# Kernel optimization log

Hardware: AMD Instinct MI355X
Metric: run time of the kernel (lower is better)

## Reference

```python
import jax, jax.numpy as jnp
import numpy as np

ALPHA = 0.15
N_PROPAGATION = 5
N_NODES = 100000
N_EDGES = 1600000
N_CLASSES = 50


def setup_inputs() -> dict:
    key = jax.random.key(0)
    k1, k2, k3, k4 = jax.random.split(key, 4)
    logits = jax.random.normal(k1, (N_NODES, N_CLASSES), dtype=jnp.float32)
    edge_rows = jax.random.randint(k2, (N_EDGES,), 0, N_NODES, dtype=jnp.int32)
    edge_cols = jax.random.randint(k3, (N_EDGES,), 0, N_NODES, dtype=jnp.int32)
    edge_vals = jax.random.uniform(k4, (N_EDGES,), dtype=jnp.float32)
    return {"logits": logits, "edge_rows": edge_rows, "edge_cols": edge_cols,
            "edge_vals": edge_vals}


def reference(logits, edge_rows, edge_cols, edge_vals):
    """APPNP-style power iteration: logits <- alpha*init + (1-alpha)*A_hat@logits.

    A_hat is given as an edge list (rows=dest, cols=src, vals=weights).
    Note: the source module's per-step dropout is dead code (its result is
    discarded and the original A_hat is used in the spmm), so the effective
    math carries no dropout.
    """
    n = logits.shape[0]
    initial_logits = logits

    def step(l, _):
        # sparse A_hat @ l: gather source rows, scale by edge value, scatter-add to dest
        msg = edge_vals[:, None] * l[edge_cols]          # [E, C]
        agg = jax.ops.segment_sum(msg, edge_rows, num_segments=n)  # [N, C]
        return ALPHA * initial_logits + (1.0 - ALPHA) * agg, None

    out, _ = jax.lax.scan(step, logits, None, length=N_PROPAGATION)
    return out
```

## Files before the change

### kernel.cpp

```cpp
#include <hip/hip_runtime.h>


constexpr float ALPHA  = 0.15f;
constexpr int   NPROP  = 5;
constexpr int   NCLASS = 50;
constexpr int   C2     = 25;
constexpr int   C2P    = 32;
constexpr int   NPB    = 10;
constexpr int   NB     = 256;
constexpr int   PB     = 256;
constexpr int   RBSH   = 9;

__device__ __forceinline__ unsigned f2bf(float x) {
    unsigned u = __float_as_uint(x);
    return (u + 0x7fffu + ((u >> 16) & 1u)) >> 16;
}


__global__ __launch_bounds__(256) void reduce_chunk(const int* __restrict__ counts,
                                                    int* __restrict__ bs, int n) {
    __shared__ int tsum[256];
    int b = blockIdx.x, t = threadIdx.x;
    int chunk = (n + gridDim.x - 1) / gridDim.x;
    int blo = b * chunk;
    int bhi = blo + chunk; if (bhi > n) bhi = n;
    int s = 0;
    for (int i = blo + t; i < bhi; i += 256) s += counts[i];
    tsum[t] = s;
    __syncthreads();
    for (int off = 128; off; off >>= 1) {
        if (t < off) tsum[t] += tsum[t + off];
        __syncthreads();
    }
    if (t == 0) bs[b] = tsum[0];
}

__global__ __launch_bounds__(256) void scan_blocksums(int* __restrict__ bs) {
    __shared__ int tmp[256];
    int t = threadIdx.x;
    tmp[t] = bs[t];
    __syncthreads();
    for (int off = 1; off < 256; off <<= 1) {
        int v = (t >= off) ? tmp[t - off] : 0;
        __syncthreads();
        tmp[t] += v;
        __syncthreads();
    }
    bs[t] = t ? tmp[t - 1] : 0;
}

__global__ __launch_bounds__(256) void scan_chunk(int* __restrict__ counts,
                                                  const int* __restrict__ bs,
                                                  int* __restrict__ offs,
                                                  int n, int E) {
    __shared__ int tsum[256];
    int b = blockIdx.x, t = threadIdx.x;
    int chunk = (n + gridDim.x - 1) / gridDim.x;
    int blo = b * chunk;
    int bhi = blo + chunk; if (bhi > n) bhi = n;
    int per = (chunk + 255) / 256;
    int lo = blo + t * per;
    int hi = lo + per;
    if (lo > bhi) lo = bhi;
    if (hi > bhi) hi = bhi;
    int s = 0;
    for (int i = lo; i < hi; ++i) s += counts[i];
    tsum[t] = s;
    __syncthreads();
    for (int off = 1; off < 256; off <<= 1) {
        int v = (t >= off) ? tsum[t - off] : 0;
        __syncthreads();
        tsum[t] += v;
        __syncthreads();
    }
    int run = bs[b] + (t ? tsum[t - 1] : 0);
    for (int i = lo; i < hi; ++i) {
        int v = counts[i];
        offs[i] = run;
        run += v;
    }
    if (b == 0 && t == 0) offs[n] = E;
}


__global__ __launch_bounds__(256) void part_hist(const int* __restrict__ rows,
                                                 int* __restrict__ blockhist, int E) {
    __shared__ int h[NB];
    int b = blockIdx.x, t = threadIdx.x;
    h[t] = 0;
    __syncthreads();
    int chunk = (E + gridDim.x - 1) / gridDim.x;
    int lo = b * chunk;
    int hi = lo + chunk; if (hi > E) hi = E;
    for (int i = lo + t; i < hi; i += 256) atomicAdd(&h[rows[i] >> RBSH], 1);
    __syncthreads();
    blockhist[t * PB + b] = h[t];
}

__global__ __launch_bounds__(256) void part_scatter(const int* __restrict__ rows,
                                                    const int* __restrict__ cols,
                                                    const float* __restrict__ vals,
                                                    const int* __restrict__ bh_scanned,
                                                    int2* __restrict__ recbuf, int E) {
    __shared__ int cur[NB];
    int b = blockIdx.x, t = threadIdx.x;
    cur[t] = bh_scanned[t * PB + b];
    __syncthreads();
    int chunk = (E + gridDim.x - 1) / gridDim.x;
    int lo = b * chunk;
    int hi = lo + chunk; if (hi > E) hi = E;
    for (int i = lo + t; i < hi; i += 256) {
        int r  = rows[i];
        int bk = r >> RBSH;
        int p  = atomicAdd(&cur[bk], 1);
        int2 rec;
        rec.x = ((r & ((1 << RBSH) - 1)) << 17) | cols[i];
        rec.y = __float_as_int(vals[i]);
        recbuf[p] = rec;
    }
}

__global__ __launch_bounds__(256) void bucket_csr(const int2* __restrict__ recbuf,
                                                  const int* __restrict__ bh_scanned,
                                                  int* __restrict__ offs,
                                                  int2* __restrict__ epack,
                                                  int N, int E) {
    __shared__ int cnt[512];
    __shared__ int ex[512];
    __shared__ int pair[256];
    int b = blockIdx.x, t = threadIdx.x;
    int rowlo = b << RBSH;
    int nrows = N - rowlo; if (nrows > (1 << RBSH)) nrows = (1 << RBSH);
    int bstart = bh_scanned[b * PB];
    int bend   = (b == gridDim.x - 1) ? E : bh_scanned[(b + 1) * PB];

    cnt[t] = 0; cnt[t + 256] = 0;
    __syncthreads();
    for (int k = bstart + t; k < bend; k += 256)
        atomicAdd(&cnt[recbuf[k].x >> 17], 1);
    __syncthreads();

    int c0 = cnt[2 * t], c1 = cnt[2 * t + 1];
    pair[t] = c0 + c1;
    __syncthreads();
    for (int off = 1; off < 256; off <<= 1) {
        int v = (t >= off) ? pair[t - off] : 0;
        __syncthreads();
        pair[t] += v;
        __syncthreads();
    }
    int pbase = t ? pair[t - 1] : 0;
    ex[2 * t]     = pbase;
    ex[2 * t + 1] = pbase + c0;
    __syncthreads();

    if (t < nrows)        offs[rowlo + t]       = bstart + ex[t];
    if (t + 256 < nrows)  offs[rowlo + t + 256] = bstart + ex[t + 256];
    if (t == 0 && rowlo + nrows == N) offs[N] = E;

    for (int k = bstart + t; k < bend; k += 256) {
        int2 rec = recbuf[k];
        int lr  = rec.x >> 17;
        int col = rec.x & 0x1FFFF;
        int p   = bstart + atomicAdd(&ex[lr], 1);
        int2 e; e.x = col; e.y = rec.y;
        epack[p] = e;
    }
}


__global__ __launch_bounds__(256) void to_bf16_kernel(const float* __restrict__ logits,
                                                      unsigned* __restrict__ lbf, int N) {
    int i = blockIdx.x * blockDim.x + threadIdx.x;
    int stride = gridDim.x * blockDim.x;
    int total = N << 5;
    const float2* l2 = (const float2*)logits;
    for (; i < total; i += stride) {
        int node = i >> 5;
        int c = i & 31;
        unsigned v = 0;
        if (c < C2) {
            float2 lv = l2[node * C2 + c];
            v = f2bf(lv.x) | (f2bf(lv.y) << 16);
        }
        lbf[i] = v;
    }
}


__global__ __launch_bounds__(256) void spmm_bf_kernel(
    const unsigned* __restrict__ lbf, const float* __restrict__ init,
    const int* __restrict__ offs, const int2* __restrict__ epack,
    unsigned* __restrict__ obf, float* __restrict__ of32, int n, int final_f32) {
    int t = threadIdx.x;
    if (t >= NPB * C2) return;
    int node = blockIdx.x * NPB + t / C2;
    if (node >= n) return;
    int c = t % C2;
    int beg = offs[node], end = offs[node + 1];
    float ax0 = 0.f, ay0 = 0.f, ax1 = 0.f, ay1 = 0.f;
    int k = beg;
    for (; k + 4 <= end; k += 4) {
        int2 e0 = epack[k];
        int2 e1 = epack[k + 1];
        int2 e2 = epack[k + 2];
        int2 e3 = epack[k + 3];
        unsigned u0 = lbf[(e0.x << 5) + c];
        unsigned u1 = lbf[(e1.x << 5) + c];
        unsigned u2 = lbf[(e2.x << 5) + c];
        unsigned u3 = lbf[(e3.x << 5) + c];
        float v0 = __int_as_float(e0.y);
        float v1 = __int_as_float(e1.y);
        float v2 = __int_as_float(e2.y);
        float v3 = __int_as_float(e3.y);
        ax0 = fmaf(v0, __uint_as_float(u0 << 16), ax0);
        ay0 = fmaf(v0, __uint_as_float(u0 & 0xffff0000u), ay0);
        ax1 = fmaf(v1, __uint_as_float(u1 << 16), ax1);
        ay1 = fmaf(v1, __uint_as_float(u1 & 0xffff0000u), ay1);
        ax0 = fmaf(v2, __uint_as_float(u2 << 16), ax0);
        ay0 = fmaf(v2, __uint_as_float(u2 & 0xffff0000u), ay0);
        ax1 = fmaf(v3, __uint_as_float(u3 << 16), ax1);
        ay1 = fmaf(v3, __uint_as_float(u3 & 0xffff0000u), ay1);
    }
    for (; k < end; ++k) {
        int2 e = epack[k];
        unsigned u = lbf[(e.x << 5) + c];
        float v = __int_as_float(e.y);
        ax0 = fmaf(v, __uint_as_float(u << 16), ax0);
        ay0 = fmaf(v, __uint_as_float(u & 0xffff0000u), ay0);
    }
    float ax = ax0 + ax1, ay = ay0 + ay1;
    float2 iv = ((const float2*)init)[node * C2 + c];
    float ox = ALPHA * iv.x + (1.0f - ALPHA) * ax;
    float oy = ALPHA * iv.y + (1.0f - ALPHA) * ay;
    if (final_f32) {
        float2 o; o.x = ox; o.y = oy;
        ((float2*)of32)[node * C2 + c] = o;
    } else {
        obf[(node << 5) + c] = f2bf(ox) | (f2bf(oy) << 16);
    }
}


__global__ void zero_f32(float* __restrict__ p, int n) {
    int i = blockIdx.x * blockDim.x + threadIdx.x;
    int stride = gridDim.x * blockDim.x;
    for (; i < n; i += stride) p[i] = 0.0f;
}

__global__ __launch_bounds__(256) void scatter_kernel(
    const float* __restrict__ l, const int* __restrict__ rows,
    const int* __restrict__ cols, const float* __restrict__ vals,
    float* __restrict__ agg, int E) {
    long long gid = (long long)blockIdx.x * blockDim.x + threadIdx.x;
    int e = (int)(gid >> 6);
    if (e >= E) return;
    int c = (int)(gid & 63);
    if (c >= NCLASS) return;
    float m = vals[e] * l[(long long)cols[e] * NCLASS + c];
    atomicAdd(&agg[(long long)rows[e] * NCLASS + c], m);
}

__global__ void combine_kernel(const float* __restrict__ init,
                               const float* __restrict__ agg,
                               float* __restrict__ out, int n) {
    int i = blockIdx.x * blockDim.x + threadIdx.x;
    int stride = gridDim.x * blockDim.x;
    for (; i < n; i += stride)
        out[i] = ALPHA * init[i] + (1.0f - ALPHA) * agg[i];
}


static inline size_t align_up(size_t x, size_t a) { return (x + a - 1) & ~(a - 1); }

extern "C" void kernel_launch(void* const* d_in, const int* in_sizes, int n_in,
                              void* d_out, int out_size, void* d_ws, size_t ws_size,
                              hipStream_t stream) {
    const float* logits = (const float*)d_in[0];
    const int*   rows   = (const int*)d_in[1];
    const int*   cols   = (const int*)d_in[2];
    const float* vals   = (const float*)d_in[3];
    float* out = (float*)d_out;

    const int E  = in_sizes[1];
    const int NC = out_size;
    const int N  = NC / NCLASS;

    const int NBPB = NB * PB;

    size_t rec_bytes  = (size_t)E * 8;
    size_t lbf_bytes  = (size_t)N * C2P * 4;
    size_t shared_sz  = rec_bytes > lbf_bytes ? rec_bytes : lbf_bytes;

    size_t off_bh     = 0;
    size_t off_bs     = align_up(off_bh   + (size_t)(NBPB + 1) * 4, 256);
    size_t off_offs   = align_up(off_bs   + (size_t)256 * 4,        256);
    size_t off_shared = align_up(off_offs + (size_t)(N + 1) * 4,    256);
    size_t off_epack  = align_up(off_shared + shared_sz,            256);
    size_t off_lbfa   = align_up(off_epack  + (size_t)E * 8,        256);
    size_t need       = off_lbfa + lbf_bytes;

    bool fits = (N <= (NB << RBSH)) && (N <= (1 << 17)) && (ws_size >= need);

    if (fits) {
        char* ws = (char*)d_ws;
        int*      bh     = (int*)     (ws + off_bh);
        int*      bs     = (int*)     (ws + off_bs);
        int*      offs   = (int*)     (ws + off_offs);
        int2*     recbuf = (int2*)    (ws + off_shared);
        unsigned* lbf_b  = (unsigned*)(ws + off_shared);
        int2*     epack  = (int2*)    (ws + off_epack);
        unsigned* lbf_a  = (unsigned*)(ws + off_lbfa);

        int nbuckets = (N + (1 << RBSH) - 1) >> RBSH;

        part_hist<<<PB, 256, 0, stream>>>(rows, bh, E);
        reduce_chunk<<<256, 256, 0, stream>>>(bh, bs, NBPB);
        scan_blocksums<<<1, 256, 0, stream>>>(bs);
        scan_chunk<<<256, 256, 0, stream>>>(bh, bs, bh, NBPB, E);
        part_scatter<<<PB, 256, 0, stream>>>(rows, cols, vals, bh, recbuf, E);
        bucket_csr<<<nbuckets, 256, 0, stream>>>(recbuf, bh, offs, epack, N, E);
        to_bf16_kernel<<<2048, 256, 0, stream>>>(logits, lbf_a, N);

        int sblocks = (N + NPB - 1) / NPB;
        unsigned* cur = lbf_a;
        unsigned* nxt = lbf_b;
        for (int it = 0; it < NPROP; ++it) {
            int fin = (it == NPROP - 1);
            spmm_bf_kernel<<<sblocks, 256, 0, stream>>>(
                cur, logits, offs, epack, nxt, out, N, fin);
            unsigned* tmp = cur; cur = nxt; nxt = tmp;
        }
    } else {
        float* agg = (float*)d_ws;
        long long sthreads = (long long)E * 64;
        int sblocks = (int)((sthreads + 255) / 256);
        int cblocks = (NC + 255) / 256;
        const float* cur = logits;
        for (int it = 0; it < NPROP; ++it) {
            zero_f32<<<2048, 256, 0, stream>>>(agg, NC);
            scatter_kernel<<<sblocks, 256, 0, stream>>>(cur, rows, cols, vals, agg, E);
            combine_kernel<<<cblocks, 256, 0, stream>>>(logits, agg, out, NC);
            cur = out;
        }
    }
}
```

Baseline: 273.3 us.

## Sort nodes by in-degree to balance SpMM work within blocks

Adds a counting sort of nodes by CSR degree (histogram, scan, scatter) to build a permutation. Each SpMM block then processes nodes of similar degree, which cuts wavefront divergence from unequal loop trip counts. The cost is three extra small kernels plus a memset. Node order within a block also becomes scattered, so writes and offs reads lose locality.

Result: slower. 542.1 us (+98.3%).

```diff
diff --git a/kernel.cpp b/kernel.cpp
--- a/kernel.cpp
+++ b/kernel.cpp
@@ -10,6 +10,7 @@
 constexpr int   NB     = 256;
 constexpr int   PB     = 256;
 constexpr int   RBSH   = 9;
+constexpr int   DBINS  = 64;
 
 __device__ __forceinline__ unsigned f2bf(float x) {
     unsigned u = __float_as_uint(x);
@@ -169,6 +170,51 @@
 }
 
 
+__global__ __launch_bounds__(256) void deg_hist(const int* __restrict__ offs,
+                                                int* __restrict__ dhist, int N) {
+    __shared__ int h[DBINS];
+    int t = threadIdx.x;
+    if (t < DBINS) h[t] = 0;
+    __syncthreads();
+    int i = blockIdx.x * blockDim.x + t;
+    int stride = gridDim.x * blockDim.x;
+    for (; i < N; i += stride) {
+        int d = offs[i + 1] - offs[i];
+        if (d > DBINS - 1) d = DBINS - 1;
+        atomicAdd(&h[d], 1);
+    }
+    __syncthreads();
+    if (t < DBINS && h[t]) atomicAdd(&dhist[t], h[t]);
+}
+
+__global__ void deg_scan(const int* __restrict__ dhist, int* __restrict__ dcur) {
+    __shared__ int tmp[DBINS];
+    int t = threadIdx.x;
+    tmp[t] = dhist[t];
+    __syncthreads();
+    for (int off = 1; off < DBINS; off <<= 1) {
+        int v = (t >= off) ? tmp[t - off] : 0;
+        __syncthreads();
+        tmp[t] += v;
+        __syncthreads();
+    }
+    dcur[t] = t ? tmp[t - 1] : 0;
+}
+
+__global__ __launch_bounds__(256) void deg_scatter(const int* __restrict__ offs,
+                                                   int* __restrict__ dcur,
+                                                   int* __restrict__ perm, int N) {
+    int i = blockIdx.x * blockDim.x + threadIdx.x;
+    int stride = gridDim.x * blockDim.x;
+    for (; i < N; i += stride) {
+        int d = offs[i + 1] - offs[i];
+        if (d > DBINS - 1) d = DBINS - 1;
+        int p = atomicAdd(&dcur[d], 1);
+        perm[p] = i;
+    }
+}
+
+
 __global__ __launch_bounds__(256) void to_bf16_kernel(const float* __restrict__ logits,
                                                       unsigned* __restrict__ lbf, int N) {
     int i = blockIdx.x * blockDim.x + threadIdx.x;
@@ -191,11 +237,13 @@
 __global__ __launch_bounds__(256) void spmm_bf_kernel(
     const unsigned* __restrict__ lbf, const float* __restrict__ init,
     const int* __restrict__ offs, const int2* __restrict__ epack,
+    const int* __restrict__ perm,
     unsigned* __restrict__ obf, float* __restrict__ of32, int n, int final_f32) {
     int t = threadIdx.x;
     if (t >= NPB * C2) return;
-    int node = blockIdx.x * NPB + t / C2;
-    if (node >= n) return;
+    int g = blockIdx.x * NPB + t / C2;
+    if (g >= n) return;
+    int node = perm[g];
     int c = t % C2;
     int beg = offs[node], end = offs[node + 1];
     float ax0 = 0.f, ay0 = 0.f, ax1 = 0.f, ay1 = 0.f;
@@ -295,7 +343,9 @@
     size_t off_bh     = 0;
     size_t off_bs     = align_up(off_bh   + (size_t)(NBPB + 1) * 4, 256);
     size_t off_offs   = align_up(off_bs   + (size_t)256 * 4,        256);
-    size_t off_shared = align_up(off_offs + (size_t)(N + 1) * 4,    256);
+    size_t off_perm   = align_up(off_offs + (size_t)(N + 1) * 4,    256);
+    size_t off_dh     = align_up(off_perm + (size_t)N * 4,          256);
+    size_t off_shared = align_up(off_dh   + (size_t)(2 * DBINS) * 4, 256);
     size_t off_epack  = align_up(off_shared + shared_sz,            256);
     size_t off_lbfa   = align_up(off_epack  + (size_t)E * 8,        256);
     size_t need       = off_lbfa + lbf_bytes;
@@ -307,6 +357,9 @@
         int*      bh     = (int*)     (ws + off_bh);
         int*      bs     = (int*)     (ws + off_bs);
         int*      offs   = (int*)     (ws + off_offs);
+        int*      perm   = (int*)     (ws + off_perm);
+        int*      dhist  = (int*)     (ws + off_dh);
+        int*      dcur   = dhist + DBINS;
         int2*     recbuf = (int2*)    (ws + off_shared);
         unsigned* lbf_b  = (unsigned*)(ws + off_shared);
         int2*     epack  = (int2*)    (ws + off_epack);
@@ -320,6 +373,13 @@
         scan_chunk<<<256, 256, 0, stream>>>(bh, bs, bh, NBPB, E);
         part_scatter<<<PB, 256, 0, stream>>>(rows, cols, vals, bh, recbuf, E);
         bucket_csr<<<nbuckets, 256, 0, stream>>>(recbuf, bh, offs, epack, N, E);
+
+        hipMemsetAsync(dhist, 0, 2 * DBINS * sizeof(int), stream);
+        int nblk = (N + 255) / 256; if (nblk > 1024) nblk = 1024;
+        deg_hist<<<nblk, 256, 0, stream>>>(offs, dhist, N);
+        deg_scan<<<1, DBINS, 0, stream>>>(dhist, dcur);
+        deg_scatter<<<nblk, 256, 0, stream>>>(offs, dcur, perm, N);
+
         to_bf16_kernel<<<2048, 256, 0, stream>>>(logits, lbf_a, N);
 
         int sblocks = (N + NPB - 1) / NPB;
@@ -328,7 +388,7 @@
         for (int it = 0; it < NPROP; ++it) {
             int fin = (it == NPROP - 1);
             spmm_bf_kernel<<<sblocks, 256, 0, stream>>>(
-                cur, logits, offs, epack, nxt, out, N, fin);
+                cur, logits, offs, epack, perm, nxt, out, N, fin);
             unsigned* tmp = cur; cur = nxt; nxt = tmp;
         }
     } else {
```

## Sort nodes by in-degree so SpMM blocks get balanced row lengths

Applied to the files above, without the earlier changes.

Adds a counting sort of nodes by in-degree (capped at 63) using a histogram, the existing scan kernels, and a scatter into a permutation array. The SpMM kernel then processes nodes in permuted order, so the ten nodes in each block have similar degrees. This is meant to cut intra-block divergence and tail imbalance. It costs five extra preprocessing launches and an indirect perm lookup, and output writes follow permuted order, which is less coalesced.

New measurement: 280.2 us. 2.5% more time.

```diff
diff --git a/kernel.cpp b/kernel.cpp
--- a/kernel.cpp
+++ b/kernel.cpp
@@ -10,6 +10,8 @@
 constexpr int   NB     = 256;
 constexpr int   PB     = 256;
 constexpr int   RBSH   = 9;
+constexpr int   DBINS  = 64;
+constexpr int   DPB    = 256;
 
 __device__ __forceinline__ unsigned f2bf(float x) {
     unsigned u = __float_as_uint(x);
@@ -165,6 +167,43 @@
         int p   = bstart + atomicAdd(&ex[lr], 1);
         int2 e; e.x = col; e.y = rec.y;
         epack[p] = e;
+    }
+}
+
+
+__global__ __launch_bounds__(256) void deg_hist2(const int* __restrict__ offs,
+                                                 int* __restrict__ dbh, int N) {
+    __shared__ int h[DBINS];
+    int b = blockIdx.x, t = threadIdx.x;
+    if (t < DBINS) h[t] = 0;
+    __syncthreads();
+    int chunk = (N + gridDim.x - 1) / gridDim.x;
+    int lo = b * chunk;
+    int hi = lo + chunk; if (hi > N) hi = N;
+    for (int i = lo + t; i < hi; i += 256) {
+        int d = offs[i + 1] - offs[i];
+        if (d > DBINS - 1) d = DBINS - 1;
+        atomicAdd(&h[d], 1);
+    }
+    __syncthreads();
+    if (t < DBINS) dbh[t * DPB + b] = h[t];
+}
+
+__global__ __launch_bounds__(256) void deg_scatter2(const int* __restrict__ offs,
+                                                    const int* __restrict__ dbh_scanned,
+                                                    int* __restrict__ perm, int N) {
+    __shared__ int cur[DBINS];
+    int b = blockIdx.x, t = threadIdx.x;
+    if (t < DBINS) cur[t] = dbh_scanned[t * DPB + b];
+    __syncthreads();
+    int chunk = (N + gridDim.x - 1) / gridDim.x;
+    int lo = b * chunk;
+    int hi = lo + chunk; if (hi > N) hi = N;
+    for (int i = lo + t; i < hi; i += 256) {
+        int d = offs[i + 1] - offs[i];
+        if (d > DBINS - 1) d = DBINS - 1;
+        int p = atomicAdd(&cur[d], 1);
+        perm[p] = i;
     }
 }
 
@@ -191,11 +230,13 @@
 __global__ __launch_bounds__(256) void spmm_bf_kernel(
     const unsigned* __restrict__ lbf, const float* __restrict__ init,
     const int* __restrict__ offs, const int2* __restrict__ epack,
+    const int* __restrict__ perm,
     unsigned* __restrict__ obf, float* __restrict__ of32, int n, int final_f32) {
     int t = threadIdx.x;
     if (t >= NPB * C2) return;
-    int node = blockIdx.x * NPB + t / C2;
-    if (node >= n) return;
+    int g = blockIdx.x * NPB + t / C2;
+    if (g >= n) return;
+    int node = perm[g];
     int c = t % C2;
     int beg = offs[node], end = offs[node + 1];
     float ax0 = 0.f, ay0 = 0.f, ax1 = 0.f, ay1 = 0.f;
@@ -295,7 +336,8 @@
     size_t off_bh     = 0;
     size_t off_bs     = align_up(off_bh   + (size_t)(NBPB + 1) * 4, 256);
     size_t off_offs   = align_up(off_bs   + (size_t)256 * 4,        256);
-    size_t off_shared = align_up(off_offs + (size_t)(N + 1) * 4,    256);
+    size_t off_perm   = align_up(off_offs + (size_t)(N + 1) * 4,    256);
+    size_t off_shared = align_up(off_perm + (size_t)N * 4,          256);
     size_t off_epack  = align_up(off_shared + shared_sz,            256);
     size_t off_lbfa   = align_up(off_epack  + (size_t)E * 8,        256);
     size_t need       = off_lbfa + lbf_bytes;
@@ -307,6 +349,7 @@
         int*      bh     = (int*)     (ws + off_bh);
         int*      bs     = (int*)     (ws + off_bs);
         int*      offs   = (int*)     (ws + off_offs);
+        int*      perm   = (int*)     (ws + off_perm);
         int2*     recbuf = (int2*)    (ws + off_shared);
         unsigned* lbf_b  = (unsigned*)(ws + off_shared);
         int2*     epack  = (int2*)    (ws + off_epack);
@@ -320,6 +363,14 @@
         scan_chunk<<<256, 256, 0, stream>>>(bh, bs, bh, NBPB, E);
         part_scatter<<<PB, 256, 0, stream>>>(rows, cols, vals, bh, recbuf, E);
         bucket_csr<<<nbuckets, 256, 0, stream>>>(recbuf, bh, offs, epack, N, E);
+
+        const int DBT = DBINS * DPB;
+        deg_hist2<<<DPB, 256, 0, stream>>>(offs, bh, N);
+        reduce_chunk<<<256, 256, 0, stream>>>(bh, bs, DBT);
+        scan_blocksums<<<1, 256, 0, stream>>>(bs);
+        scan_chunk<<<256, 256, 0, stream>>>(bh, bs, bh, DBT, N);
+        deg_scatter2<<<DPB, 256, 0, stream>>>(offs, bh, perm, N);
+
         to_bf16_kernel<<<2048, 256, 0, stream>>>(logits, lbf_a, N);
 
         int sblocks = (N + NPB - 1) / NPB;
@@ -328,7 +379,7 @@
         for (int it = 0; it < NPROP; ++it) {
             int fin = (it == NPROP - 1);
             spmm_bf_kernel<<<sblocks, 256, 0, stream>>>(
-                cur, logits, offs, epack, nxt, out, N, fin);
+                cur, logits, offs, epack, perm, nxt, out, N, fin);
             unsigned* tmp = cur; cur = nxt; nxt = tmp;
         }
     } else {
```
